# Performance work log

Measured on AMD Instinct MI355X. Metric: run time of the kernel, lower is better.

Reference implementation:

```python
import jax, jax.numpy as jnp
import numpy as np

HIDDEN = 1024
HEADS = 16
HEAD_DIM = HIDDEN // HEADS


def setup_inputs() -> dict:
    key = jax.random.key(0)
    ks = jax.random.split(key, 7)
    B, S, H = 8, 1024, HIDDEN
    hidden_states = jax.random.normal(ks[0], (B, S, H), dtype=jnp.float32)
    attention_mask = jnp.zeros((B, 1, 1, S), dtype=jnp.float32)
    # Xavier-uniform weights [out, in], zero biases (matches module init)
    limit = float(np.sqrt(6.0 / (H + H)))
    Wq = jax.random.uniform(ks[1], (H, H), minval=-limit, maxval=limit, dtype=jnp.float32)
    Wk = jax.random.uniform(ks[2], (H, H), minval=-limit, maxval=limit, dtype=jnp.float32)
    Wv = jax.random.uniform(ks[3], (H, H), minval=-limit, maxval=limit, dtype=jnp.float32)
    bq = jnp.zeros((H,), dtype=jnp.float32)
    bk = jnp.zeros((H,), dtype=jnp.float32)
    bv = jnp.zeros((H,), dtype=jnp.float32)
    return {"hidden_states": hidden_states, "attention_mask": attention_mask,
            "Wq": Wq, "bq": bq, "Wk": Wk, "bk": bk, "Wv": Wv, "bv": bv}


def _split_heads(x):
    # [B, S, H] -> [B, heads, S, head_dim]
    B, S, _ = x.shape
    return x.reshape(B, S, HEADS, HEAD_DIM).transpose(0, 2, 1, 3)


def reference(hidden_states, attention_mask, Wq, bq, Wk, bk, Wv, bv):
    # Linear projections: y = x @ W^T + b  (weights stored [out, in] as in torch)
    q = _split_heads(hidden_states @ Wq.T + bq)
    k = _split_heads(hidden_states @ Wk.T + bk)
    v = _split_heads(hidden_states @ Wv.T + bv)
    scale = 1.0 / (HEAD_DIM ** 0.5)
    scores = jnp.einsum('bhqd,bhkd->bhqk', q, k) * scale  # [B,heads,S,S]
    scores = scores + attention_mask
    probs = jax.nn.softmax(scores, axis=-1)
    # dropout is identity at inference
    ctx = jnp.einsum('bhqk,bhkd->bhqd', probs, v)
    B, _, S, _ = ctx.shape
    return ctx.transpose(0, 2, 1, 3).reshape(B, S, HIDDEN)
```

## Files before the change

kernel.cpp:

```cpp
#include <hip/hip_runtime.h>
#include <hip/hip_bf16.h>
#include <stdint.h>

#define B_ 8
#define S_ 1024
#define NH_ 16
#define D_ 64
#define H_ 1024
#define M_TOT (B_*S_)
#define LOG2E 1.44269504088896f

typedef __attribute__((ext_vector_type(8))) short short8;
typedef __attribute__((ext_vector_type(4))) float f32x4;
typedef __attribute__((ext_vector_type(16))) float f32x16;

#if __has_builtin(__builtin_amdgcn_exp2f)
#define EXP2(x) __builtin_amdgcn_exp2f(x)
#else
#define EXP2(x) __expf((x) * 0.69314718056f)
#endif

static __device__ __forceinline__ unsigned short f2bf(float f) {
  union { float f; unsigned u; } c; c.f = f;
  unsigned u = c.u;
  return (unsigned short)((u + 0x7fffu + ((u >> 16) & 1u)) >> 16);
}

static __device__ __forceinline__ void gld_lds16(void* lds, const void* g) {
  __builtin_amdgcn_global_load_lds((const __attribute__((address_space(1))) unsigned*)g,
                                   (__attribute__((address_space(3))) unsigned*)lds, 16, 0, 0);
}

#define WAIT_LGKM0()  asm volatile("s_waitcnt lgkmcnt(0)" ::: "memory")
#define WAIT_VM(n)    asm volatile("s_waitcnt vmcnt(" #n ")" ::: "memory")
#define SBAR()        __builtin_amdgcn_s_barrier()
#define SCHED0()      __builtin_amdgcn_sched_barrier(0)
#define PRIO1()       __builtin_amdgcn_s_setprio(1)
#define PRIO0()       __builtin_amdgcn_s_setprio(0)

__global__ void cvt_f32_bf16(const float* __restrict__ X,
                             const float* __restrict__ Wq,
                             const float* __restrict__ Wk,
                             const float* __restrict__ Wv,
                             unsigned short* __restrict__ Xbf,
                             unsigned short* __restrict__ Wbf) {
  const long long NX = (long long)M_TOT * H_;
  const long long NW = (long long)H_ * H_;
  long long t = (long long)blockIdx.x * blockDim.x + threadIdx.x;
  const long long stride = (long long)gridDim.x * blockDim.x;
  const long long total4 = (NX + 3 * NW) >> 2;
  for (; t < total4; t += stride) {
    long long e = t << 2;
    const float* src; unsigned short* dst;
    if (e < NX) { src = X + e; dst = Xbf + e; }
    else {
      long long r = e - NX;
      int w = (int)(r / NW);
      long long o = r - (long long)w * NW;
      src = (w == 0 ? Wq : (w == 1 ? Wk : Wv)) + o;
      dst = Wbf + (long long)w * NW + o;
    }
    float4 v = *(const float4*)src;
    ushort4 u;
    u.x = f2bf(v.x); u.y = f2bf(v.y); u.z = f2bf(v.z); u.w = f2bf(v.w);
    *(ushort4*)dst = u;
  }
}

#define QBM 256
#define QBN 256
#define QBK 64
#define ABYTES 32768
#define BUFSZ  65536

#define MMQ(I0, J0, AF, BF)                                               \
  _Pragma("unroll")                                                       \
  for (int a_ = 0; a_ < 4; ++a_)                                          \
    _Pragma("unroll")                                                     \
    for (int b_ = 0; b_ < 2; ++b_)                                        \
      _Pragma("unroll")                                                   \
      for (int k_ = 0; k_ < 2; ++k_)                                      \
        acc[(I0) + a_][(J0) + b_] = __builtin_amdgcn_mfma_f32_16x16x32_bf16( \
            AF[a_][k_], BF[b_][k_], acc[(I0) + a_][(J0) + b_], 0, 0, 0);

#define RD_A(BUF, MH)                                                     \
  _Pragma("unroll")                                                       \
  for (int f_ = 0; f_ < 4; ++f_)                                          \
    _Pragma("unroll")                                                     \
    for (int k_ = 0; k_ < 2; ++k_) A[f_][k_] = rdA(BUF, MH, f_, k_);

#define RD_B(DST, BUF, NH)                                                \
  _Pragma("unroll")                                                       \
  for (int f_ = 0; f_ < 2; ++f_)                                          \
    _Pragma("unroll")                                                     \
    for (int k_ = 0; k_ < 2; ++k_) DST[f_][k_] = rdB(BUF, NH, f_, k_);

__global__ __launch_bounds__(512, 1) void qkv_gemm(
    const unsigned short* __restrict__ Xbf,
    const unsigned short* __restrict__ Wbf,
    const float* __restrict__ bq, const float* __restrict__ bk,
    const float* __restrict__ bv,
    unsigned short* __restrict__ Qo, unsigned short* __restrict__ Ko,
    unsigned short* __restrict__ Vt) {
  __shared__ char lds[2 * BUFSZ];

  const int tid = threadIdx.x;
  const int w = tid >> 6;
  const int l = tid & 63;
  const int lrow = l & 15, lgrp = l >> 4;
  const int wm = w >> 2, wn = w & 3;

  const int orig = blockIdx.x;
  const int xcd = orig & 7;
  const int slot = orig >> 3;
  const int nz = slot >> 2;
  const int mtile = (xcd * 4 + (slot & 3)) * QBM;
  const int ntile = (nz & 3) * QBN;
  const int z = nz >> 2;

  const unsigned short* Wz = Wbf + (long long)z * H_ * H_;

  const int srow = l >> 3;
  const int sslot = l & 7;
  auto stageA = [&](char* buf, int j, int k0) {
    int row = j * 8 + srow;
    int so = (sslot ^ (row & 7)) * 8;
    gld_lds16(buf + j * 1024, Xbf + (long long)(mtile + row) * H_ + k0 + so);
  };
  auto stageB = [&](char* buf, int j, int k0) {
    int row = j * 8 + srow;
    int so = (sslot ^ (row & 7)) * 8;
    gld_lds16(buf + ABYTES + j * 1024, Wz + (long long)(ntile + row) * H_ + k0 + so);
  };

  const int offA = (z == 2) ? ABYTES : 0;
  const int offB = (z == 2) ? 0 : ABYTES;
  auto rdA = [&](const char* buf, int mh, int fi, int ks) -> short8 {
    int r = wm * 128 + mh * 64 + fi * 16 + lrow;
    return *(const short8*)(buf + offA + r * 128 + (((ks * 4 + lgrp) ^ (r & 7)) * 16));
  };
  auto rdB = [&](const char* buf, int nh, int fi, int ks) -> short8 {
    int r = wn * 64 + nh * 32 + fi * 16 + lrow;
    return *(const short8*)(buf + offB + r * 128 + (((ks * 4 + lgrp) ^ (r & 7)) * 16));
  };

  f32x4 acc[8][4];
  f32x4 zero = {0.f, 0.f, 0.f, 0.f};
  #pragma unroll
  for (int a = 0; a < 8; ++a)
    #pragma unroll
    for (int c = 0; c < 4; ++c) acc[a][c] = zero;

  short8 A[4][2], B0[2][2], B1[2][2];

  #pragma unroll
  for (int c = 0; c < 4; ++c) stageA(lds, w * 4 + c, 0);
  #pragma unroll
  for (int c = 0; c < 4; ++c) stageB(lds, w * 4 + c, 0);
  SCHED0(); WAIT_VM(0); SCHED0();
  SBAR();

  #pragma unroll 1
  for (int t = 0; t < 16; ++t) {
    char* buf  = lds + ((t & 1) ? BUFSZ : 0);
    char* nbuf = lds + ((t & 1) ? 0 : BUFSZ);
    const bool st = (t < 15);
    const int k0n = (t + 1) * QBK;

    RD_A(buf, 0);
    RD_B(B0, buf, 0);
    if (st) {
      stageA(nbuf, w * 4 + 0, k0n); stageA(nbuf, w * 4 + 1, k0n);
      stageA(nbuf, w * 4 + 2, k0n); stageA(nbuf, w * 4 + 3, k0n);
    }
    SBAR();
    WAIT_LGKM0(); SCHED0();
    PRIO1(); MMQ(0, 0, A, B0); PRIO0();
    SBAR();

    RD_B(B1, buf, 1);
    if (st) {
      stageB(nbuf, w * 4 + 0, k0n); stageB(nbuf, w * 4 + 1, k0n);
      stageB(nbuf, w * 4 + 2, k0n); stageB(nbuf, w * 4 + 3, k0n);
    }
    SBAR();
    WAIT_LGKM0(); SCHED0();
    PRIO1(); MMQ(0, 2, A, B1); PRIO0();
    SBAR();

    RD_A(buf, 1);
    SBAR();
    WAIT_LGKM0(); SCHED0();
    PRIO1(); MMQ(4, 2, A, B1); PRIO0();
    SBAR();

    PRIO1(); MMQ(4, 0, A, B0); PRIO0();
    if (st) { SCHED0(); WAIT_VM(0); SCHED0(); }
    SBAR();
  }

  const float* bias = (z == 0) ? bq : (z == 1) ? bk : bv;
  if (z != 2) {
    unsigned short* O = (z == 0) ? Qo : Ko;
    #pragma unroll
    for (int in = 0; in < 4; ++in) {
      int n = ntile + wn * 64 + in * 16 + lrow;
      float bv_ = bias[n];
      int h = n >> 6, d = n & 63;
      #pragma unroll
      for (int im = 0; im < 8; ++im)
        #pragma unroll
        for (int r = 0; r < 4; ++r) {
          int m = mtile + wm * 128 + im * 16 + lgrp * 4 + r;
          float val = acc[im][in][r] + bv_;
          if (z == 0) val *= 0.125f * LOG2E;
          int b = m >> 10, s = m & 1023;
          O[(((long long)(b * NH_ + h)) * S_ + s) * D_ + d] = f2bf(val);
        }
    }
  } else {
    #pragma unroll
    for (int im = 0; im < 8; ++im)
      #pragma unroll
      for (int r = 0; r < 4; ++r) {
        int nfull = ntile + wm * 128 + im * 16 + lgrp * 4 + r;
        float bv_ = bias[nfull];
        int h = nfull >> 6, d = nfull & 63;
        #pragma unroll
        for (int in = 0; in < 4; ++in) {
          int mfull = mtile + wn * 64 + in * 16 + lrow;
          float val = acc[im][in][r] + bv_;
          int b = mfull >> 10, s = mfull & 1023;
          Vt[(((long long)(b * NH_ + h)) * D_ + d) * S_ + s] = f2bf(val);
        }
      }
  }
}

__global__ __launch_bounds__(256, 2) void attn_fused(
    const unsigned short* __restrict__ Qbf,
    const unsigned short* __restrict__ Kbf,
    const unsigned short* __restrict__ Vtb,
    const float* __restrict__ mask,
    float* __restrict__ out) {
  __shared__ char lds[32768];
  const int tid = threadIdx.x, w = tid >> 6, l = tid & 63;
  const int l31 = l & 31, h = l >> 5;

  const int lid = blockIdx.x;
  const int xcd = lid & 7, k8 = lid >> 3;
  const int bh = xcd * 16 + (k8 >> 2);
  const int qt = k8 & 3;
  const int b = bh >> 4, hd = bh & 15;
  const int q0 = qt * 256 + w * 64;

  const unsigned short* Kg = Kbf + (long long)bh * S_ * D_;
  const unsigned short* Vg = Vtb + (long long)bh * D_ * S_;
  const float* mrow = mask + b * S_;

  {
    const int row = (w * 2) * 8 + (l >> 3);
    const int row1 = (w * 2 + 1) * 8 + (l >> 3);
    const int so = ((l & 7) ^ (row & 7)) * 8;
    const int so1 = ((l & 7) ^ (row1 & 7)) * 8;
    gld_lds16(lds + (w * 2) * 1024,        Kg + (long long)row * D_ + so);
    gld_lds16(lds + (w * 2 + 1) * 1024,    Kg + (long long)row1 * D_ + so1);
    gld_lds16(lds + 8192 + (w * 2) * 1024, Vg + (long long)row * S_ + so);
    gld_lds16(lds + 8192 + (w * 2 + 1) * 1024, Vg + (long long)row1 * S_ + so1);
  }

  short8 qf[2][4];
  #pragma unroll
  for (int qb = 0; qb < 2; ++qb)
    #pragma unroll
    for (int ks = 0; ks < 4; ++ks)
      qf[qb][ks] = *(const short8*)(Qbf + ((long long)bh * S_ + q0 + qb * 32 + l31) * D_ + ks * 16 + 8 * h);

  f32x16 acc[2][2];
  #pragma unroll
  for (int db = 0; db < 2; ++db)
    #pragma unroll
    for (int qb = 0; qb < 2; ++qb)
      #pragma unroll
      for (int r = 0; r < 16; ++r) acc[db][qb][r] = 0.f;
  float m_run[2] = {-1e30f, -1e30f};
  float l_run[2] = {0.f, 0.f};

  __syncthreads();

  for (int kt = 0; kt < S_ / 64; ++kt) {
    const int p = kt & 1;
    char* ldsK = lds + p * 16384;
    char* ldsV = ldsK + 8192;
    const int key0 = kt * 64;

    if (kt < S_ / 64 - 1) {
      char* nb = lds + (p ^ 1) * 16384;
      const int nk0 = key0 + 64;
      #pragma unroll
      for (int t = 0; t < 2; ++t) {
        int j = w * 2 + t;
        int row = j * 8 + (l >> 3);
        int so = ((l & 7) ^ (row & 7)) * 8;
        gld_lds16(nb + j * 1024,        Kg + (long long)(nk0 + row) * D_ + so);
        gld_lds16(nb + 8192 + j * 1024, Vg + (long long)row * S_ + nk0 + so);
      }
    }

    f32x16 sc[2][2];
    #pragma unroll
    for (int kb = 0; kb < 2; ++kb)
      #pragma unroll
      for (int qb = 0; qb < 2; ++qb)
        #pragma unroll
        for (int r = 0; r < 16; ++r) sc[kb][qb][r] = 0.f;

    #pragma unroll
    for (int kb = 0; kb < 2; ++kb) {
      short8 kf[4];
      #pragma unroll
      for (int ks = 0; ks < 4; ++ks) {
        int row = kb * 32 + l31;
        int g = (2 * ks + h) ^ (row & 7);
        kf[ks] = *(const short8*)(ldsK + row * 128 + g * 16);
      }
      __builtin_amdgcn_s_setprio(1);
      #pragma unroll
      for (int qb = 0; qb < 2; ++qb)
        #pragma unroll
        for (int ks = 0; ks < 4; ++ks)
          sc[kb][qb] = __builtin_amdgcn_mfma_f32_32x32x16_bf16(
              kf[ks], qf[qb][ks], sc[kb][qb], 0, 0, 0);
      __builtin_amdgcn_s_setprio(0);
    }

    short8 pfrag[2][4];
    #pragma unroll
    for (int qb = 0; qb < 2; ++qb) {
      float sv[32];
      #pragma unroll
      for (int kb = 0; kb < 2; ++kb)
        #pragma unroll
        for (int rg = 0; rg < 4; ++rg) {
          f32x4 m4 = *(const f32x4*)(mrow + key0 + kb * 32 + rg * 8 + 4 * h);
          #pragma unroll
          for (int c = 0; c < 4; ++c)
            sv[kb * 16 + rg * 4 + c] = fmaf(m4[c], LOG2E, sc[kb][qb][rg * 4 + c]);
        }
      float r16[16];
      #pragma unroll
      for (int i = 0; i < 16; ++i) r16[i] = fmaxf(sv[i], sv[i + 16]);
      #pragma unroll
      for (int i = 0; i < 8; ++i) r16[i] = fmaxf(r16[i], r16[i + 8]);
      #pragma unroll
      for (int i = 0; i < 4; ++i) r16[i] = fmaxf(r16[i], r16[i + 4]);
      float pm = fmaxf(fmaxf(r16[0], r16[1]), fmaxf(r16[2], r16[3]));
      pm = fmaxf(pm, __shfl_xor(pm, 32));
      if (!__all(pm - m_run[qb] <= 11.5f)) {
        float mn = fmaxf(m_run[qb], pm);
        float rs = EXP2(m_run[qb] - mn);
        m_run[qb] = mn;
        l_run[qb] *= rs;
        #pragma unroll
        for (int db = 0; db < 2; ++db)
          #pragma unroll
          for (int r = 0; r < 16; ++r) acc[db][qb][r] *= rs;
      }
      const float mcur = m_run[qb];
      #pragma unroll
      for (int i = 0; i < 32; ++i) sv[i] = EXP2(sv[i] - mcur);
      #pragma unroll
      for (int i = 0; i < 16; ++i) r16[i] = sv[i] + sv[i + 16];
      #pragma unroll
      for (int i = 0; i < 8; ++i) r16[i] = r16[i] + r16[i + 8];
      #pragma unroll
      for (int i = 0; i < 4; ++i) r16[i] = r16[i] + r16[i + 4];
      float ps = (r16[0] + r16[1]) + (r16[2] + r16[3]);
      ps += __shfl_xor(ps, 32);
      l_run[qb] += ps;

      unsigned Wd[8][2];
      #pragma unroll
      for (int j = 0; j < 8; ++j) {
        int base = (j >> 2) * 16 + (j & 3) * 4;
        asm("v_cvt_pk_bf16_f32 %0, %1, %2" : "=v"(Wd[j][0]) : "v"(sv[base + 0]), "v"(sv[base + 1]));
        asm("v_cvt_pk_bf16_f32 %0, %1, %2" : "=v"(Wd[j][1]) : "v"(sv[base + 2]), "v"(sv[base + 3]));
      }
      #pragma unroll
      for (int ks = 0; ks < 4; ++ks) {
        unsigned s0 = h ? Wd[2 * ks][0] : Wd[2 * ks + 1][0];
        unsigned s1 = h ? Wd[2 * ks][1] : Wd[2 * ks + 1][1];
        unsigned r0 = __shfl_xor(s0, 32);
        unsigned r1 = __shfl_xor(s1, 32);
        unsigned o0 = h ? Wd[2 * ks + 1][0] : Wd[2 * ks][0];
        unsigned o1 = h ? Wd[2 * ks + 1][1] : Wd[2 * ks][1];
        union { unsigned u[4]; short8 s; } fu;
        fu.u[0] = h ? r0 : o0;
        fu.u[1] = h ? r1 : o1;
        fu.u[2] = h ? o0 : r0;
        fu.u[3] = h ? o1 : r1;
        pfrag[qb][ks] = fu.s;
      }
    }

    #pragma unroll
    for (int db = 0; db < 2; ++db) {
      short8 vf[4];
      #pragma unroll
      for (int ks = 0; ks < 4; ++ks) {
        int row = db * 32 + l31;
        int g = (2 * ks + h) ^ (row & 7);
        vf[ks] = *(const short8*)(ldsV + row * 128 + g * 16);
      }
      __builtin_amdgcn_s_setprio(1);
      #pragma unroll
      for (int qb = 0; qb < 2; ++qb)
        #pragma unroll
        for (int ks = 0; ks < 4; ++ks)
          acc[db][qb] = __builtin_amdgcn_mfma_f32_32x32x16_bf16(
              vf[ks], pfrag[qb][ks], acc[db][qb], 0, 0, 0);
      __builtin_amdgcn_s_setprio(0);
    }

    __syncthreads();
  }

  #pragma unroll
  for (int qb = 0; qb < 2; ++qb) {
    float inv = 1.0f / l_run[qb];
    int q = q0 + qb * 32 + l31;
    float* orow = out + ((long long)b * S_ + q) * H_ + hd * D_;
    #pragma unroll
    for (int db = 0; db < 2; ++db)
      #pragma unroll
      for (int rg = 0; rg < 4; ++rg) {
        f32x4 v4;
        #pragma unroll
        for (int c = 0; c < 4; ++c) v4[c] = acc[db][qb][rg * 4 + c] * inv;
        *(f32x4*)(orow + db * 32 + rg * 8 + 4 * h) = v4;
      }
  }
}

extern "C" void kernel_launch(void* const* d_in, const int* in_sizes, int n_in,
                              void* d_out, int out_size, void* d_ws, size_t ws_size,
                              hipStream_t stream) {
  const float* X    = (const float*)d_in[0];
  const float* mask = (const float*)d_in[1];
  const float* Wq   = (const float*)d_in[2];
  const float* bq   = (const float*)d_in[3];
  const float* Wk   = (const float*)d_in[4];
  const float* bk   = (const float*)d_in[5];
  const float* Wv   = (const float*)d_in[6];
  const float* bv   = (const float*)d_in[7];
  float* out = (float*)d_out;

  char* ws = (char*)d_ws;
  unsigned short* Xbf = (unsigned short*)ws;
  unsigned short* Wbf = (unsigned short*)(ws + 16777216);
  unsigned short* Qb  = (unsigned short*)(ws + 23068672);
  unsigned short* Kb  = (unsigned short*)(ws + 39845888);
  unsigned short* Vt  = (unsigned short*)(ws + 56623104);

  hipLaunchKernelGGL(cvt_f32_bf16, dim3(2048), dim3(256), 0, stream,
                     X, Wq, Wk, Wv, Xbf, Wbf);
  hipLaunchKernelGGL(qkv_gemm, dim3(384), dim3(512), 0, stream,
                     Xbf, Wbf, bq, bk, bv, Qb, Kb, Vt);
  hipLaunchKernelGGL(attn_fused, dim3(512), dim3(256), 0, stream,
                     Qb, Kb, Vt, mask, out);
}
```

Measured before the change: 138.2 us.

## Deepen GEMM and attention load pipelines, stage mask in LDS

The QKV GEMM now stages operands in half-tiles interleaved with the MFMA phases, keeping one half-tile prefetched ahead and using partial vmcnt waits instead of draining all loads each iteration. The attention kernel switches from double to triple buffering of K/V tiles with partial waits and bare barriers. It also loads the mask row into LDS once rather than reading it from global memory every tile. The aim is to hide global load latency better, at the cost of more LDS use and fragile waitcnt accounting.

```diff
diff --git a/kernel.cpp b/kernel.cpp
--- a/kernel.cpp
+++ b/kernel.cpp
@@ -31,12 +31,12 @@
                                    (__attribute__((address_space(3))) unsigned*)lds, 16, 0, 0);
 }
 
-#define WAIT_LGKM0()  asm volatile("s_waitcnt lgkmcnt(0)" ::: "memory")
-#define WAIT_VM(n)    asm volatile("s_waitcnt vmcnt(" #n ")" ::: "memory")
-#define SBAR()        __builtin_amdgcn_s_barrier()
-#define SCHED0()      __builtin_amdgcn_sched_barrier(0)
-#define PRIO1()       __builtin_amdgcn_s_setprio(1)
-#define PRIO0()       __builtin_amdgcn_s_setprio(0)
+#define WAIT_LGKM0() asm volatile("s_waitcnt lgkmcnt(0)" ::: "memory")
+#define WAIT_VM(n)   asm volatile("s_waitcnt vmcnt(" #n ")" ::: "memory")
+#define SBAR()       __builtin_amdgcn_s_barrier()
+#define SCHED0()     __builtin_amdgcn_sched_barrier(0)
+#define PRIO1()      __builtin_amdgcn_s_setprio(1)
+#define PRIO0()      __builtin_amdgcn_s_setprio(0)
 
 __global__ void cvt_f32_bf16(const float* __restrict__ X,
                              const float* __restrict__ Wq,
@@ -70,8 +70,8 @@
 #define QBM 256
 #define QBN 256
 #define QBK 64
-#define ABYTES 32768
-#define BUFSZ  65536
+#define REG_B 32768
+#define BUFSZ 65536
 
 #define MMQ(I0, J0, AF, BF)                                               \
   _Pragma("unroll")                                                       \
@@ -83,17 +83,17 @@
         acc[(I0) + a_][(J0) + b_] = __builtin_amdgcn_mfma_f32_16x16x32_bf16( \
             AF[a_][k_], BF[b_][k_], acc[(I0) + a_][(J0) + b_], 0, 0, 0);
 
-#define RD_A(BUF, MH)                                                     \
+#define RD_A(BUF, MS)                                                     \
   _Pragma("unroll")                                                       \
   for (int f_ = 0; f_ < 4; ++f_)                                          \
     _Pragma("unroll")                                                     \
-    for (int k_ = 0; k_ < 2; ++k_) A[f_][k_] = rdA(BUF, MH, f_, k_);
-
-#define RD_B(DST, BUF, NH)                                                \
+    for (int k_ = 0; k_ < 2; ++k_) A[f_][k_] = rdA(BUF, MS, f_, k_);
+
+#define RD_B(DST, BUF, NS)                                                \
   _Pragma("unroll")                                                       \
   for (int f_ = 0; f_ < 2; ++f_)                                          \
     _Pragma("unroll")                                                     \
-    for (int k_ = 0; k_ < 2; ++k_) DST[f_][k_] = rdB(BUF, NH, f_, k_);
+    for (int k_ = 0; k_ < 2; ++k_) DST[f_][k_] = rdB(BUF, NS, f_, k_);
 
 __global__ __launch_bounds__(512, 1) void qkv_gemm(
     const unsigned short* __restrict__ Xbf,
@@ -122,25 +122,31 @@
 
   const int srow = l >> 3;
   const int sslot = l & 7;
-  auto stageA = [&](char* buf, int j, int k0) {
-    int row = j * 8 + srow;
-    int so = (sslot ^ (row & 7)) * 8;
-    gld_lds16(buf + j * 1024, Xbf + (long long)(mtile + row) * H_ + k0 + so);
+  auto stageReg = [&](char* buf, int region, int half, int k0) {
+    #pragma unroll
+    for (int jj = 0; jj < 2; ++jj) {
+      int j = w * 2 + jj;
+      int row = half * 128 + j * 8 + srow;
+      int so = (sslot ^ (row & 7)) * 8;
+      if (region == 0)
+        gld_lds16(buf + (half * 16 + j) * 1024,
+                  Xbf + (long long)(mtile + row) * H_ + k0 + so);
+      else
+        gld_lds16(buf + REG_B + (half * 16 + j) * 1024,
+                  Wz + (long long)(ntile + row) * H_ + k0 + so);
+    }
   };
-  auto stageB = [&](char* buf, int j, int k0) {
-    int row = j * 8 + srow;
-    int so = (sslot ^ (row & 7)) * 8;
-    gld_lds16(buf + ABYTES + j * 1024, Wz + (long long)(ntile + row) * H_ + k0 + so);
-  };
-
-  const int offA = (z == 2) ? ABYTES : 0;
-  const int offB = (z == 2) ? 0 : ABYTES;
-  auto rdA = [&](const char* buf, int mh, int fi, int ks) -> short8 {
-    int r = wm * 128 + mh * 64 + fi * 16 + lrow;
+  auto stageOpA = [&](char* buf, int half, int k0) { stageReg(buf, (z == 2) ? 1 : 0, half, k0); };
+  auto stageOpB = [&](char* buf, int half, int k0) { stageReg(buf, (z == 2) ? 0 : 1, half, k0); };
+
+  const int offA = (z == 2) ? REG_B : 0;
+  const int offB = (z == 2) ? 0 : REG_B;
+  auto rdA = [&](const char* buf, int ms, int fi, int ks) -> short8 {
+    int r = ms * 128 + wm * 64 + fi * 16 + lrow;
     return *(const short8*)(buf + offA + r * 128 + (((ks * 4 + lgrp) ^ (r & 7)) * 16));
   };
-  auto rdB = [&](const char* buf, int nh, int fi, int ks) -> short8 {
-    int r = wn * 64 + nh * 32 + fi * 16 + lrow;
+  auto rdB = [&](const char* buf, int ns, int fj, int ks) -> short8 {
+    int r = ns * 128 + wn * 32 + fj * 16 + lrow;
     return *(const short8*)(buf + offB + r * 128 + (((ks * 4 + lgrp) ^ (r & 7)) * 16));
   };
 
@@ -153,66 +159,80 @@
 
   short8 A[4][2], B0[2][2], B1[2][2];
 
-  #pragma unroll
-  for (int c = 0; c < 4; ++c) stageA(lds, w * 4 + c, 0);
-  #pragma unroll
-  for (int c = 0; c < 4; ++c) stageB(lds, w * 4 + c, 0);
+  stageOpA(lds, 0, 0);
+  stageOpB(lds, 0, 0);
+  stageOpB(lds, 1, 0);
+  stageOpA(lds, 1, 0);
+  stageOpA(lds + BUFSZ, 0, QBK);
+  SCHED0(); WAIT_VM(6); SCHED0();
+  SBAR();
+
+  #pragma unroll 1
+  for (int t = 0; t < 15; ++t) {
+    char* bc = lds + ((t & 1) ? BUFSZ : 0);
+    char* bn = lds + ((t & 1) ? 0 : BUFSZ);
+    const int k1 = (t + 1) * QBK;
+    const int k2 = (t + 2) * QBK;
+    const bool st2 = (t + 2 < 16);
+
+    RD_A(bc, 0);
+    RD_B(B0, bc, 0);
+    stageOpB(bn, 0, k1);
+    WAIT_LGKM0(); SCHED0();
+    PRIO1(); MMQ(0, 0, A, B0); PRIO0();
+    SCHED0(); WAIT_VM(6); SCHED0();
+    SBAR();
+
+    RD_B(B1, bc, 1);
+    stageOpB(bn, 1, k1);
+    WAIT_LGKM0(); SCHED0();
+    PRIO1(); MMQ(0, 2, A, B1); PRIO0();
+    SCHED0(); WAIT_VM(6); SCHED0();
+    SBAR();
+
+    RD_A(bc, 1);
+    stageOpA(bn, 1, k1);
+    WAIT_LGKM0(); SCHED0();
+    PRIO1(); MMQ(4, 2, A, B1); PRIO0();
+    SCHED0(); WAIT_VM(6); SCHED0();
+    SBAR();
+
+    if (st2) stageOpA(bc, 0, k2);
+    PRIO1(); MMQ(4, 0, A, B0); PRIO0();
+    SCHED0(); WAIT_VM(6); SCHED0();
+    SBAR();
+  }
+
   SCHED0(); WAIT_VM(0); SCHED0();
   SBAR();
-
-  #pragma unroll 1
-  for (int t = 0; t < 16; ++t) {
-    char* buf  = lds + ((t & 1) ? BUFSZ : 0);
-    char* nbuf = lds + ((t & 1) ? 0 : BUFSZ);
-    const bool st = (t < 15);
-    const int k0n = (t + 1) * QBK;
-
-    RD_A(buf, 0);
-    RD_B(B0, buf, 0);
-    if (st) {
-      stageA(nbuf, w * 4 + 0, k0n); stageA(nbuf, w * 4 + 1, k0n);
-      stageA(nbuf, w * 4 + 2, k0n); stageA(nbuf, w * 4 + 3, k0n);
-    }
-    SBAR();
+  {
+    char* bc = lds + BUFSZ;
+    RD_A(bc, 0);
+    RD_B(B0, bc, 0);
     WAIT_LGKM0(); SCHED0();
     PRIO1(); MMQ(0, 0, A, B0); PRIO0();
-    SBAR();
-
-    RD_B(B1, buf, 1);
-    if (st) {
-      stageB(nbuf, w * 4 + 0, k0n); stageB(nbuf, w * 4 + 1, k0n);
-      stageB(nbuf, w * 4 + 2, k0n); stageB(nbuf, w * 4 + 3, k0n);
-    }
-    SBAR();
+    RD_B(B1, bc, 1);
     WAIT_LGKM0(); SCHED0();
     PRIO1(); MMQ(0, 2, A, B1); PRIO0();
-    SBAR();
-
-    RD_A(buf, 1);
-    SBAR();
-    WAIT_LGKM0(); SCHED0();
-    PRIO1(); MMQ(4, 2, A, B1); PRIO0();
-    SBAR();
-
-    PRIO1(); MMQ(4, 0, A, B0); PRIO0();
-    if (st) { SCHED0(); WAIT_VM(0); SCHED0(); }
-    SBAR();
+    RD_A(bc, 1);
+    WAIT_LGKM0(); SCHED0();
+    PRIO1(); MMQ(4, 2, A, B1); MMQ(4, 0, A, B0); PRIO0();
   }
 
   const float* bias = (z == 0) ? bq : (z == 1) ? bk : bv;
   if (z != 2) {
     unsigned short* O = (z == 0) ? Qo : Ko;
     #pragma unroll
-    for (int in = 0; in < 4; ++in) {
-      int n = ntile + wn * 64 + in * 16 + lrow;
+    for (int nj = 0; nj < 4; ++nj) {
+      int n = ntile + (nj >> 1) * 128 + wn * 32 + (nj & 1) * 16 + lrow;
       float bv_ = bias[n];
       int h = n >> 6, d = n & 63;
       #pragma unroll
-      for (int im = 0; im < 8; ++im)
+      for (int mi = 0; mi < 8; ++mi)
         #pragma unroll
         for (int r = 0; r < 4; ++r) {
-          int m = mtile + wm * 128 + im * 16 + lgrp * 4 + r;
-          float val = acc[im][in][r] + bv_;
+          int m = mtile + (mi >> 2) * 128 + wm * 64 + (mi & 3) * 16 + lgrp * 4 + r;
+          float val = acc[mi][nj][r] + bv_;
           if (z == 0) val *= 0.125f * LOG2E;
           int b = m >> 10, s = m & 1023;
           O[(((long long)(b * NH_ + h)) * S_ + s) * D_ + d] = f2bf(val);
@@ -220,16 +240,16 @@
     }
   } else {
     #pragma unroll
-    for (int im = 0; im < 8; ++im)
+    for (int mi = 0; mi < 8; ++mi)
       #pragma unroll
       for (int r = 0; r < 4; ++r) {
-        int nfull = ntile + wm * 128 + im * 16 + lgrp * 4 + r;
+        int nfull = ntile + (mi >> 2) * 128 + wm * 64 + (mi & 3) * 16 + lgrp * 4 + r;
         float bv_ = bias[nfull];
         int h = nfull >> 6, d = nfull & 63;
         #pragma unroll
-        for (int in = 0; in < 4; ++in) {
-          int mfull = mtile + wn * 64 + in * 16 + lrow;
-          float val = acc[im][in][r] + bv_;
+        for (int nj = 0; nj < 4; ++nj) {
+          int mfull = mtile + (nj >> 1) * 128 + wn * 32 + (nj & 1) * 16 + lrow;
+          float val = acc[mi][nj][r] + bv_;
           int b = mfull >> 10, s = mfull & 1023;
           Vt[(((long long)(b * NH_ + h)) * D_ + d) * S_ + s] = f2bf(val);
         }
@@ -243,7 +263,8 @@
     const unsigned short* __restrict__ Vtb,
     const float* __restrict__ mask,
     float* __restrict__ out) {
-  __shared__ char lds[32768];
+  __shared__ char lds[3 * 16384 + 4096];
+  char* ldsM = lds + 49152;
   const int tid = threadIdx.x, w = tid >> 6, l = tid & 63;
   const int l31 = l & 31, h = l >> 5;
 
@@ -258,16 +279,17 @@
   const unsigned short* Vg = Vtb + (long long)bh * D_ * S_;
   const float* mrow = mask + b * S_;
 
-  {
-    const int row = (w * 2) * 8 + (l >> 3);
-    const int row1 = (w * 2 + 1) * 8 + (l >> 3);
-    const int so = ((l & 7) ^ (row & 7)) * 8;
-    const int so1 = ((l & 7) ^ (row1 & 7)) * 8;
-    gld_lds16(lds + (w * 2) * 1024,        Kg + (long long)row * D_ + so);
-    gld_lds16(lds + (w * 2 + 1) * 1024,    Kg + (long long)row1 * D_ + so1);
-    gld_lds16(lds + 8192 + (w * 2) * 1024, Vg + (long long)row * S_ + so);
-    gld_lds16(lds + 8192 + (w * 2 + 1) * 1024, Vg + (long long)row1 * S_ + so1);
-  }
+  auto stageKV = [&](int kt, char* buf) {
+    const int key0 = kt * 64;
+    #pragma unroll
+    for (int t = 0; t < 2; ++t) {
+      int j = w * 2 + t;
+      int row = j * 8 + (l >> 3);
+      int so = ((l & 7) ^ (row & 7)) * 8;
+      gld_lds16(buf + j * 1024,        Kg + (long long)(key0 + row) * D_ + so);
+      gld_lds16(buf + 8192 + j * 1024, Vg + (long long)row * S_ + key0 + so);
+    }
+  };
 
   short8 qf[2][4];
   #pragma unroll
@@ -275,6 +297,13 @@
     #pragma unroll
     for (int ks = 0; ks < 4; ++ks)
       qf[qb][ks] = *(const short8*)(Qbf + ((long long)bh * S_ + q0 + qb * 32 + l31) * D_ + ks * 16 + 8 * h);
+  gld_lds16(ldsM + w * 1024, mrow + w * 256 + l * 4);
+  SCHED0(); WAIT_VM(0); SCHED0();
+
+  stageKV(0, lds);
+  stageKV(1, lds + 16384);
+  SCHED0(); WAIT_VM(4); SCHED0();
+  SBAR();
 
   f32x16 acc[2][2];
   #pragma unroll
@@ -286,26 +315,14 @@
   float m_run[2] = {-1e30f, -1e30f};
   float l_run[2] = {0.f, 0.f};
 
-  __syncthreads();
-
+  #pragma unroll 1
   for (int kt = 0; kt < S_ / 64; ++kt) {
-    const int p = kt & 1;
-    char* ldsK = lds + p * 16384;
+    char* ldsK = lds + (kt % 3) * 16384;
     char* ldsV = ldsK + 8192;
     const int key0 = kt * 64;
-
-    if (kt < S_ / 64 - 1) {
-      char* nb = lds + (p ^ 1) * 16384;
-      const int nk0 = key0 + 64;
-      #pragma unroll
-      for (int t = 0; t < 2; ++t) {
-        int j = w * 2 + t;
-        int row = j * 8 + (l >> 3);
-        int so = ((l & 7) ^ (row & 7)) * 8;
-        gld_lds16(nb + j * 1024,        Kg + (long long)(nk0 + row) * D_ + so);
-        gld_lds16(nb + 8192 + j * 1024, Vg + (long long)row * S_ + nk0 + so);
-      }
-    }
+    const bool st = (kt + 2 < S_ / 64);
+
+    if (st) stageKV(kt + 2, lds + ((kt + 2) % 3) * 16384);
 
     f32x16 sc[2][2];
     #pragma unroll
@@ -342,7 +359,7 @@
       for (int kb = 0; kb < 2; ++kb)
         #pragma unroll
         for (int rg = 0; rg < 4; ++rg) {
-          f32x4 m4 = *(const f32x4*)(mrow + key0 + kb * 32 + rg * 8 + 4 * h);
+          f32x4 m4 = *(const f32x4*)(ldsM + (key0 + kb * 32 + rg * 8 + 4 * h) * 4);
           #pragma unroll
           for (int c = 0; c < 4; ++c)
             sv[kb * 16 + rg * 4 + c] = fmaf(m4[c], LOG2E, sc[kb][qb][rg * 4 + c]);
@@ -422,7 +439,9 @@
       __builtin_amdgcn_s_setprio(0);
     }
 
-    __syncthreads();
+    if (st) { SCHED0(); WAIT_VM(4); SCHED0(); }
+    else if (kt + 1 < S_ / 64) { SCHED0(); WAIT_VM(0); SCHED0(); }
+    SBAR();
   }
 
   #pragma unroll
```

New measurement: 127.5 us. 1.08x faster.
